# Performance work log

Measured on AMD Instinct MI355X. Metric: run time of the kernel, lower is better.

## Reference

```python
import jax, jax.numpy as jnp
import numpy as np

NS, NC, T, NB = 32, 16, 64, 512
NSC = NS + NC


def setup_inputs() -> dict:
    key = jax.random.key(0)
    k1, k2, k3, k4, k5 = jax.random.split(key, 5)
    # SPD cost matrices so Quu is invertible (as assumed by the LQR math)
    L = jax.random.normal(k1, (NB, T, NSC, NSC), jnp.float32) * 0.1
    Q = L @ jnp.swapaxes(L, -1, -2) + jnp.eye(NSC, dtype=jnp.float32)
    p = jax.random.normal(k2, (NB, T, NSC), jnp.float32)
    x_init = jax.random.normal(k3, (NB, NS), jnp.float32)
    # stable-ish LTI dynamics
    A = 0.9 * jnp.eye(NS, dtype=jnp.float32) + 0.01 * jax.random.normal(k4, (NS, NS), jnp.float32)
    B = 0.1 * jax.random.normal(k5, (NS, NC), jnp.float32)
    dt = jnp.float32(0.1)
    return {"x_init": x_init, "Q": Q, "p": p, "A": A, "B": B, "dt": dt}


def _lqr(x_init, Q, p, A, B):
    ns, nc = A.shape[0], B.shape[1]
    nb, Th = Q.shape[0], Q.shape[1]
    dtype = Q.dtype

    # --- nominal rollout with zero control: x_{t+1} = A x_t ---
    def roll(x, _):
        return x @ A.T, x
    _, cx = jax.lax.scan(roll, x_init, None, length=Th)   # [T,B,ns] states x_0..x_{T-1}
    cu = jnp.zeros((Th, nb, nc), dtype)                    # current_u = 0
    xu = jnp.concatenate([cx, cu], -1)                     # [T,B,nsc]

    Qs = jnp.swapaxes(Q, 0, 1)                             # [T,B,nsc,nsc]
    ps = jnp.swapaxes(p, 0, 1)                             # [T,B,nsc]
    p_new = jnp.einsum('tbij,tbj->tbi', Qs, xu) + ps       # [T,B,nsc]

    F = jnp.concatenate([A, B], axis=1)                    # [ns, nsc]

    # --- backward Riccati recursion (V=v=0 at t=T-1 makes Qt=Q[T-1]) ---
    def bwd(carry, inp):
        V, v = carry                                       # [B,ns,ns], [B,ns]
        Qt_in, qt_in = inp
        Qt = Qt_in + jnp.einsum('si,bst,tj->bij', F, V, F)
        qt = qt_in + v @ F                                 # F^T v
        Qxx, Qxu = Qt[:, :ns, :ns], Qt[:, :ns, ns:]
        Qux, Quu = Qt[:, ns:, :ns], Qt[:, ns:, ns:]
        qx, qu = qt[:, :ns], qt[:, ns:]
        Quu_inv = jnp.linalg.pinv(Quu)
        Kt = -Quu_inv @ Qux                                # [B,nc,ns]
        kt = -jnp.einsum('bij,bj->bi', Quu_inv, qu)        # [B,nc]
        KtT = jnp.swapaxes(Kt, -1, -2)
        Vn = Qxx + Qxu @ Kt + KtT @ Qux + KtT @ Quu @ Kt
        vn = (qx + jnp.einsum('bij,bj->bi', Qxu, kt)
              + jnp.einsum('bij,bj->bi', KtT, qu)
              + jnp.einsum('bij,bj->bi', KtT @ Quu, kt))
        return (Vn, vn), (Kt, kt)

    V0 = jnp.zeros((nb, ns, ns), dtype)
    v0 = jnp.zeros((nb, ns), dtype)
    _, (Ks, ks) = jax.lax.scan(bwd, (V0, v0), (Qs, p_new), reverse=True)

    # --- forward rollout with feedback policy ---
    def fwd(carry, inp):
        xt, cost = carry
        Kt, kt, cxt, cut, Qt, pt = inp
        dut = jnp.einsum('bij,bj->bi', Kt, xt - cxt) + kt
        ut = dut + cut
        xut = jnp.concatenate([xt, ut], -1)
        cost = cost + 0.5 * jnp.einsum('bi,bij,bj->b', xut, Qt, xut) + (xut * pt).sum(-1)
        xn = xt @ A.T + ut @ B.T
        return (xn, cost), (xt, ut)

    (_, cost), (xs, us) = jax.lax.scan(
        fwd, (x_init, jnp.zeros(nb, dtype)), (Ks, ks, cx, cu, Qs, ps))
    x = jnp.swapaxes(xs, 0, 1)   # [B,T,ns]  (states x_0..x_{T-1}, matching x[...,:-1,:])
    u = jnp.swapaxes(us, 0, 1)   # [B,T,nc]
    return x, u, cost


def reference(x_init, Q, p, A, B, dt):
    # dt only matters for nonlinear relinearization; with constant LTI (A,B) it is unused.
    return _lqr(x_init, Q, p, A, B)
```

## Files before the change

kernel.cpp:

```cpp
#include <hip/hip_runtime.h>


#define NSd 32
#define NCd 16
#define Td 64
#define NBd 512
#define NSCd 48
#define SQS 52
#define TP 40

typedef __bf16 bf16x8 __attribute__((ext_vector_type(8)));
typedef __bf16 bf16x4 __attribute__((ext_vector_type(4)));
typedef float f32x4 __attribute__((ext_vector_type(4)));

#define MFMA16(a, b, c) __builtin_amdgcn_mfma_f32_16x16x32_bf16(a, b, c, 0, 0, 0)

#define XOFF ((size_t)0)
#define UOFF ((size_t)NBd * Td * NSd)
#define COFF (UOFF + (size_t)NBd * Td * NCd)

__device__ __forceinline__ float rdl(float v, int l) {
  return __uint_as_float(__builtin_amdgcn_readlane(__float_as_uint(v), l));
}

__device__ __forceinline__ void bar_lgkm() {
  asm volatile("s_waitcnt lgkmcnt(0)\n\ts_barrier" ::: "memory");
}

union LdsU {
  struct {
    __bf16 FTh[48][TP], FTl[48][TP];
    __bf16 Vh[32][TP], Vl[32][TP];
    __bf16 WTh[48][TP], WTl[48][TP];
    __bf16 Xh[32][TP], Xl[32][TP];
    __bf16 KTh[32][TP], KTl[32][TP];
    float Quu[16][17];
    float Qd[3][16][17];
    float qt[48];
    float vv[32];
  } bw;
  struct {
    float K2T[2][16 * 36];
    float kv2[2][16];
    float d[32];
    float xs[32];
    float uu[16];
  } fw;
};

#define SQSTORE(i, v)                            \
  do {                                           \
    int _r = (i) / 12, _c = (i) - _r * 12;       \
    *(float4*)&sQ[_r * SQS + _c * 4] = (v);      \
  } while (0)

__global__ __launch_bounds__(256, 2) void lqr_kernel(
    const float* __restrict__ x_init, const float* __restrict__ Qg,
    const float* __restrict__ pg, const float* __restrict__ Ag,
    const float* __restrict__ Bg, float* __restrict__ out,
    float* __restrict__ wsK, float* __restrict__ wskv) {
  const int b = blockIdx.x;
  const int tid = threadIdx.x;
  const int w = tid >> 6;
  const int lane = tid & 63;
  const int fn = lane & 15;
  const int quad = lane >> 4;
  const int k0 = quad * 8;

  __shared__ __attribute__((aligned(16))) float sQ[48 * SQS];
  __shared__ __attribute__((aligned(16))) float scx[Td][NSd];
  __shared__ __attribute__((aligned(16))) float sFf[NSd][SQS];
  __shared__ __attribute__((aligned(16))) LdsU U;
  __shared__ float scostp[4];

  for (int idx = tid; idx < 1536; idx += 256) {
    int i = idx / 48, j = idx - i * 48;
    sFf[i][j] = (j < 32) ? Ag[i * 32 + j] : Bg[i * 16 + (j - 32)];
  }
  for (int idx = tid; idx < 1536; idx += 256) {
    int a = idx >> 5, k = idx & 31;
    float f = (a < 32) ? Ag[k * 32 + a] : Bg[k * 16 + (a - 32)];
    __bf16 h = (__bf16)f;
    U.bw.FTh[a][k] = h;
    U.bw.FTl[a][k] = (__bf16)(f - (float)h);
  }
  for (int idx = tid; idx < 1024; idx += 256) {
    int r = idx >> 5, c = idx & 31;
    __bf16 z = (__bf16)0.f;
    U.bw.Vh[r][c] = z; U.bw.Vl[r][c] = z;
    U.bw.Xh[r][c] = z; U.bw.Xl[r][c] = z;
    U.bw.KTh[r][c] = z; U.bw.KTl[r][c] = z;
  }
  if (tid < 32) {
    scx[0][tid] = x_init[b * 32 + tid];
    U.bw.vv[tid] = 0.f;
  }
  {
    const float4* src = (const float4*)(Qg + ((size_t)b * Td + 63) * 2304);
    float4 v0 = src[tid];
    float4 v1 = src[tid + 256];
    SQSTORE(tid, v0);
    SQSTORE(tid + 256, v1);
    if (tid < 64) {
      float4 v2 = src[tid + 512];
      SQSTORE(tid + 512, v2);
    }
  }
  float ppf = 0.f;
  if (w == 3 && lane < 48) ppf = pg[((size_t)b * Td + 63) * 48 + lane];
  __syncthreads();

  if (w == 0) {
    for (int t2 = 0; t2 < Td - 1; ++t2) {
      if (lane < 32) {
        float acc = 0.f;
#pragma unroll
        for (int j = 0; j < 32; j += 4) {
          float4 a4 = *(const float4*)&sFf[lane][j];
          acc += a4.x * scx[t2][j] + a4.y * scx[t2][j + 1] +
                 a4.z * scx[t2][j + 2] + a4.w * scx[t2][j + 3];
        }
        scx[t2 + 1][lane] = acc;
      }
    }
  }
  __syncthreads();

  float cAcc = 0.f;
  float dAcc = 0.f;

  for (int t = Td - 1; t >= 0; --t) {
    float4 pf0, pf1, pf2;
    float ppfn;
    if (t > 0) {
      if (w < 3) {
        const float4* src = (const float4*)(Qg + ((size_t)b * Td + (t - 1)) * 2304);
        pf0 = src[tid];
        pf1 = src[tid + 192];
        pf2 = src[tid + 384];
      } else if (lane < 48) {
        ppfn = pg[((size_t)b * Td + t - 1) * 48 + lane];
      }
    }

    if (w < 3) {
      const int I = w;
      bf16x8 aH = *(const bf16x8*)&U.bw.FTh[16 * I + fn][k0];
      bf16x8 aL = *(const bf16x8*)&U.bw.FTl[16 * I + fn][k0];
#pragma unroll
      for (int J = 0; J < 2; ++J) {
        bf16x8 bH = *(const bf16x8*)&U.bw.Vh[16 * J + fn][k0];
        bf16x8 bL = *(const bf16x8*)&U.bw.Vl[16 * J + fn][k0];
        f32x4 acc = {0.f, 0.f, 0.f, 0.f};
        acc = MFMA16(aL, bH, acc);
        acc = MFMA16(aH, bL, acc);
        acc = MFMA16(aH, bH, acc);
#pragma unroll
        for (int r = 0; r < 4; ++r) {
          float v = acc[r];
          __bf16 h = (__bf16)v;
          U.bw.WTh[16 * I + 4 * quad + r][16 * J + fn] = h;
          U.bw.WTl[16 * I + 4 * quad + r][16 * J + fn] = (__bf16)(v - (float)h);
        }
      }
      bf16x8 wH = *(const bf16x8*)&U.bw.WTh[16 * I + fn][k0];
      bf16x8 wL = *(const bf16x8*)&U.bw.WTl[16 * I + fn][k0];
      if (I == 2) {
        bf16x8 bH = *(const bf16x8*)&U.bw.FTh[32 + fn][k0];
        bf16x8 bL = *(const bf16x8*)&U.bw.FTl[32 + fn][k0];
        f32x4 acc;
#pragma unroll
        for (int r = 0; r < 4; ++r)
          acc[r] = sQ[(32 + 4 * quad + r) * SQS + 32 + fn];
        acc = MFMA16(wL, bH, acc);
        acc = MFMA16(wH, bL, acc);
        acc = MFMA16(wH, bH, acc);
#pragma unroll
        for (int r = 0; r < 4; ++r) U.bw.Quu[4 * quad + r][fn] = acc[r];
      } else {
        {
          bf16x8 bH = *(const bf16x8*)&U.bw.FTh[16 * I + fn][k0];
          bf16x8 bL = *(const bf16x8*)&U.bw.FTl[16 * I + fn][k0];
          f32x4 acc;
#pragma unroll
          for (int r = 0; r < 4; ++r)
            acc[r] = sQ[(16 * I + 4 * quad + r) * SQS + 16 * I + fn];
          acc = MFMA16(wL, bH, acc);
          acc = MFMA16(wH, bL, acc);
          acc = MFMA16(wH, bH, acc);
#pragma unroll
          for (int r = 0; r < 4; ++r) U.bw.Qd[I * 2][4 * quad + r][fn] = acc[r];
        }
        if (I == 0) {
          bf16x8 bH = *(const bf16x8*)&U.bw.FTh[16 + fn][k0];
          bf16x8 bL = *(const bf16x8*)&U.bw.FTl[16 + fn][k0];
          f32x4 acc;
#pragma unroll
          for (int r = 0; r < 4; ++r)
            acc[r] = sQ[(4 * quad + r) * SQS + 16 + fn];
          acc = MFMA16(wL, bH, acc);
          acc = MFMA16(wH, bL, acc);
          acc = MFMA16(wH, bH, acc);
#pragma unroll
          for (int r = 0; r < 4; ++r) U.bw.Qd[1][4 * quad + r][fn] = acc[r];
        }
        {
          bf16x8 bH = *(const bf16x8*)&U.bw.FTh[32 + fn][k0];
          bf16x8 bL = *(const bf16x8*)&U.bw.FTl[32 + fn][k0];
          f32x4 acc;
#pragma unroll
          for (int r = 0; r < 4; ++r)
            acc[r] = sQ[(16 * I + 4 * quad + r) * SQS + 32 + fn];
          acc = MFMA16(wL, bH, acc);
          acc = MFMA16(wH, bL, acc);
          acc = MFMA16(wH, bH, acc);
#pragma unroll
          for (int r = 0; r < 4; ++r) {
            float v = acc[r];
            __bf16 h = (__bf16)v;
            U.bw.Xh[16 * I + 4 * quad + r][fn] = h;
            U.bw.Xl[16 * I + 4 * quad + r][fn] = (__bf16)(v - (float)h);
          }
        }
      }
    } else if (lane < 48) {
      float acc1 = ppf;
#pragma unroll
      for (int k = 0; k < 32; ++k) acc1 += sQ[k * SQS + lane] * scx[t][k];
      if (lane < 32) cAcc += 0.5f * scx[t][lane] * (acc1 + ppf);
      float acc = acc1;
#pragma unroll
      for (int k = 0; k < 32; ++k) acc += U.bw.vv[k] * sFf[k][lane];
      U.bw.qt[lane] = acc;
    }
    bar_lgkm();

    if (t > 0) {
      if (w < 3) {
        SQSTORE(tid, pf0);
        SQSTORE(tid + 192, pf1);
        SQSTORE(tid + 384, pf2);
      } else if (lane < 48) {
        ppf = ppfn;
      }
    }
    if (w == 3) {
      float rhs[16];
      if (lane < 32) {
        bf16x8 xh0 = *(const bf16x8*)&U.bw.Xh[lane][0];
        bf16x8 xh1 = *(const bf16x8*)&U.bw.Xh[lane][8];
        bf16x8 xl0 = *(const bf16x8*)&U.bw.Xl[lane][0];
        bf16x8 xl1 = *(const bf16x8*)&U.bw.Xl[lane][8];
#pragma unroll
        for (int i = 0; i < 8; ++i) {
          rhs[i] = (float)xh0[i] + (float)xl0[i];
          rhs[8 + i] = (float)xh1[i] + (float)xl1[i];
        }
      } else {
#pragma unroll
        for (int i = 0; i < 16; ++i) rhs[i] = U.bw.qt[32 + i];
      }
      float quu[16];
#pragma unroll
      for (int i = 0; i < 16; ++i) quu[i] = U.bw.Quu[i][fn];
#pragma unroll
      for (int r = 0; r < 15; ++r) {
        float inv = __builtin_amdgcn_rcpf(rdl(quu[r], r));
#pragma unroll
        for (int i = r + 1; i < 16; ++i) {
          float m = rdl(quu[i], r) * inv;
          rhs[i] -= m * rhs[r];
          quu[i] -= m * quu[r];
        }
      }
      float xx[16];
#pragma unroll
      for (int r = 15; r >= 0; --r) {
        float s = rhs[r];
#pragma unroll
        for (int c = r + 1; c < 16; ++c) s -= rdl(quu[r], c) * xx[c];
        xx[r] = s * __builtin_amdgcn_rcpf(rdl(quu[r], r));
      }
      if (lane < 32) {
        bf16x8 h0, l0, h1, l1;
#pragma unroll
        for (int u = 0; u < 8; ++u) {
          float kv = -xx[u];
          __bf16 hh = (__bf16)kv;
          h0[u] = hh; l0[u] = (__bf16)(kv - (float)hh);
          float kv2 = -xx[8 + u];
          __bf16 hh2 = (__bf16)kv2;
          h1[u] = hh2; l1[u] = (__bf16)(kv2 - (float)hh2);
        }
        *(bf16x8*)&U.bw.KTh[lane][0] = h0;
        *(bf16x8*)&U.bw.KTh[lane][8] = h1;
        *(bf16x8*)&U.bw.KTl[lane][0] = l0;
        *(bf16x8*)&U.bw.KTl[lane][8] = l1;
        float4* dst = (float4*)(wsK + (((size_t)b * Td + t) * 32 + lane) * 16);
        float4 v0 = {-xx[0], -xx[1], -xx[2], -xx[3]};
        float4 v1 = {-xx[4], -xx[5], -xx[6], -xx[7]};
        float4 v2 = {-xx[8], -xx[9], -xx[10], -xx[11]};
        float4 v3 = {-xx[12], -xx[13], -xx[14], -xx[15]};
        dst[0] = v0; dst[1] = v1; dst[2] = v2; dst[3] = v3;
      } else if (lane == 32) {
        float4* dst = (float4*)(wskv + ((size_t)b * Td + t) * 16);
        float4 v0 = {-xx[0], -xx[1], -xx[2], -xx[3]};
        float4 v1 = {-xx[4], -xx[5], -xx[6], -xx[7]};
        float4 v2 = {-xx[8], -xx[9], -xx[10], -xx[11]};
        float4 v3 = {-xx[12], -xx[13], -xx[14], -xx[15]};
        dst[0] = v0; dst[1] = v1; dst[2] = v2; dst[3] = v3;
        float s = 0.f;
#pragma unroll
        for (int i = 0; i < 16; ++i) s += U.bw.qt[32 + i] * xx[i];
        dAcc -= 0.5f * s;
      }
      {
        float acc = 0.f;
        bf16x8 xh0, xh1, xl0, xl1;
        if (lane < 32) {
          xh0 = *(const bf16x8*)&U.bw.Xh[lane][0];
          xh1 = *(const bf16x8*)&U.bw.Xh[lane][8];
          xl0 = *(const bf16x8*)&U.bw.Xl[lane][0];
          xl1 = *(const bf16x8*)&U.bw.Xl[lane][8];
          acc = U.bw.qt[lane];
        }
#pragma unroll
        for (int u = 0; u < 8; ++u) {
          float kt0 = -rdl(xx[u], 32);
          float kt1 = -rdl(xx[8 + u], 32);
          if (lane < 32) {
            acc += ((float)xh0[u] + (float)xl0[u]) * kt0;
            acc += ((float)xh1[u] + (float)xl1[u]) * kt1;
          }
        }
        if (lane < 32) U.bw.vv[lane] = acc;
      }
      {
        bf16x8 aH = *(const bf16x8*)&U.bw.Xh[fn][k0];
        bf16x8 aL = *(const bf16x8*)&U.bw.Xl[fn][k0];
        bf16x8 bH = *(const bf16x8*)&U.bw.KTh[fn][k0];
        bf16x8 bL = *(const bf16x8*)&U.bw.KTl[fn][k0];
        f32x4 acc;
#pragma unroll
        for (int r = 0; r < 4; ++r) acc[r] = U.bw.Qd[0][4 * quad + r][fn];
        acc = MFMA16(aL, bH, acc);
        acc = MFMA16(aH, bL, acc);
        acc = MFMA16(aH, bH, acc);
#pragma unroll
        for (int r = 0; r < 4; ++r) {
          float v = acc[r];
          __bf16 h = (__bf16)v;
          U.bw.Vh[4 * quad + r][fn] = h;
          U.bw.Vl[4 * quad + r][fn] = (__bf16)(v - (float)h);
        }
      }
      {
        bf16x8 aH = *(const bf16x8*)&U.bw.Xh[16 + fn][k0];
        bf16x8 aL = *(const bf16x8*)&U.bw.Xl[16 + fn][k0];
        bf16x8 bH = *(const bf16x8*)&U.bw.KTh[16 + fn][k0];
        bf16x8 bL = *(const bf16x8*)&U.bw.KTl[16 + fn][k0];
        f32x4 acc;
#pragma unroll
        for (int r = 0; r < 4; ++r) acc[r] = U.bw.Qd[2][4 * quad + r][fn];
        acc = MFMA16(aL, bH, acc);
        acc = MFMA16(aH, bL, acc);
        acc = MFMA16(aH, bH, acc);
#pragma unroll
        for (int r = 0; r < 4; ++r) {
          float v = acc[r];
          __bf16 h = (__bf16)v;
          U.bw.Vh[16 + 4 * quad + r][16 + fn] = h;
          U.bw.Vl[16 + 4 * quad + r][16 + fn] = (__bf16)(v - (float)h);
        }
      }
      {
        bf16x8 aH = *(const bf16x8*)&U.bw.Xh[fn][k0];
        bf16x8 aL = *(const bf16x8*)&U.bw.Xl[fn][k0];
        bf16x8 bH = *(const bf16x8*)&U.bw.KTh[16 + fn][k0];
        bf16x8 bL = *(const bf16x8*)&U.bw.KTl[16 + fn][k0];
        f32x4 acc;
#pragma unroll
        for (int r = 0; r < 4; ++r) acc[r] = U.bw.Qd[1][4 * quad + r][fn];
        acc = MFMA16(aL, bH, acc);
        acc = MFMA16(aH, bL, acc);
        acc = MFMA16(aH, bH, acc);
        bf16x4 th, tl;
#pragma unroll
        for (int r = 0; r < 4; ++r) {
          float v = acc[r];
          __bf16 h = (__bf16)v;
          __bf16 l = (__bf16)(v - (float)h);
          U.bw.Vh[4 * quad + r][16 + fn] = h;
          U.bw.Vl[4 * quad + r][16 + fn] = l;
          th[r] = h; tl[r] = l;
        }
        *(bf16x4*)&U.bw.Vh[16 + fn][4 * quad] = th;
        *(bf16x4*)&U.bw.Vl[16 + fn][4 * quad] = tl;
      }
    }
    bar_lgkm();
  }

  if (w == 3) {
    float rv = (lane < 32) ? cAcc : (lane == 32 ? dAcc : 0.f);
    rv += __shfl_down(rv, 32);
    rv += __shfl_down(rv, 16);
    rv += __shfl_down(rv, 8);
    rv += __shfl_down(rv, 4);
    rv += __shfl_down(rv, 2);
    rv += __shfl_down(rv, 1);
    if (lane == 0) scostp[0] = rv;
  }
  __syncthreads();

  if (w == 0) {
    {
      const float4* src = (const float4*)(wsK + ((size_t)b * Td) * 512);
      float4 ka = src[lane * 2], kb = src[lane * 2 + 1];
      int jj = lane >> 1, ib = (lane & 1) * 8;
      float* kt2 = U.fw.K2T[0];
      kt2[(ib + 0) * 36 + jj] = ka.x; kt2[(ib + 1) * 36 + jj] = ka.y;
      kt2[(ib + 2) * 36 + jj] = ka.z; kt2[(ib + 3) * 36 + jj] = ka.w;
      kt2[(ib + 4) * 36 + jj] = kb.x; kt2[(ib + 5) * 36 + jj] = kb.y;
      kt2[(ib + 6) * 36 + jj] = kb.z; kt2[(ib + 7) * 36 + jj] = kb.w;
      if (lane < 16) U.fw.kv2[0][lane] = wskv[(size_t)b * Td * 16 + lane];
    }
    float xr = (lane < 32) ? scx[0][lane] : 0.f;
    for (int t = 0; t < Td; ++t) {
      const int cur = t & 1, nxt = cur ^ 1;
      float4 pa, pb;
      float pk;
      if (t < Td - 1) {
        const float4* src = (const float4*)(wsK + ((size_t)b * Td + t + 1) * 512);
        pa = src[lane * 2];
        pb = src[lane * 2 + 1];
        if (lane < 16) pk = wskv[((size_t)b * Td + t + 1) * 16 + lane];
      }
      if (lane < 32) {
        U.fw.d[lane] = xr - scx[t][lane];
        U.fw.xs[lane] = xr;
        out[XOFF + ((size_t)b * Td + t) * 32 + lane] = xr;
      }
      if (lane < 16) {
        float uv = U.fw.kv2[cur][lane];
        const float* kr = &U.fw.K2T[cur][lane * 36];
#pragma unroll
        for (int j4 = 0; j4 < 8; ++j4) {
          float4 kk = *(const float4*)&kr[j4 * 4];
          float4 dd = *(const float4*)&U.fw.d[j4 * 4];
          uv += kk.x * dd.x + kk.y * dd.y + kk.z * dd.z + kk.w * dd.w;
        }
        U.fw.uu[lane] = uv;
        out[UOFF + ((size_t)b * Td + t) * 16 + lane] = uv;
      }
      if (lane < 32) {
        float acc = 0.f;
#pragma unroll
        for (int j4 = 0; j4 < 8; ++j4) {
          float4 ff = *(const float4*)&sFf[lane][j4 * 4];
          float4 xv = *(const float4*)&U.fw.xs[j4 * 4];
          acc += ff.x * xv.x + ff.y * xv.y + ff.z * xv.z + ff.w * xv.w;
        }
#pragma unroll
        for (int j4 = 0; j4 < 4; ++j4) {
          float4 ff = *(const float4*)&sFf[lane][32 + j4 * 4];
          float4 uv = *(const float4*)&U.fw.uu[j4 * 4];
          acc += ff.x * uv.x + ff.y * uv.y + ff.z * uv.z + ff.w * uv.w;
        }
        xr = acc;
      }
      if (t < Td - 1) {
        int jj = lane >> 1, ib = (lane & 1) * 8;
        float* kt2 = U.fw.K2T[nxt];
        kt2[(ib + 0) * 36 + jj] = pa.x; kt2[(ib + 1) * 36 + jj] = pa.y;
        kt2[(ib + 2) * 36 + jj] = pa.z; kt2[(ib + 3) * 36 + jj] = pa.w;
        kt2[(ib + 4) * 36 + jj] = pb.x; kt2[(ib + 5) * 36 + jj] = pb.y;
        kt2[(ib + 6) * 36 + jj] = pb.z; kt2[(ib + 7) * 36 + jj] = pb.w;
        if (lane < 16) U.fw.kv2[nxt][lane] = pk;
      }
    }
    if (lane == 0) out[COFF + b] = scostp[0];
  }
}

extern "C" void kernel_launch(void* const* d_in, const int* in_sizes, int n_in,
                              void* d_out, int out_size, void* d_ws, size_t ws_size,
                              hipStream_t stream) {
  const float* x_init = (const float*)d_in[0];
  const float* Qg = (const float*)d_in[1];
  const float* pg = (const float*)d_in[2];
  const float* Ag = (const float*)d_in[3];
  const float* Bg = (const float*)d_in[4];
  float* out = (float*)d_out;
  float* wsK = (float*)d_ws;
  float* wskv = wsK + (size_t)NBd * Td * NSd * NCd;
  lqr_kernel<<<NBd, 256, 0, stream>>>(x_init, Qg, pg, Ag, Bg, out, wsK, wskv);
}
```

Baseline: 636.2 us.

## Pack two batch problems per 512-thread block with shared F tables

```diff
diff --git a/kernel.cpp b/kernel.cpp
--- a/kernel.cpp
+++ b/kernel.cpp
@@ -27,100 +27,106 @@
   asm volatile("s_waitcnt lgkmcnt(0)\n\ts_barrier" ::: "memory");
 }
 
-union LdsU {
-  struct {
-    __bf16 FTh[48][TP], FTl[48][TP];
-    __bf16 Vh[32][TP], Vl[32][TP];
-    __bf16 WTh[48][TP], WTl[48][TP];
-    __bf16 Xh[32][TP], Xl[32][TP];
-    __bf16 KTh[32][TP], KTl[32][TP];
-    float Quu[16][17];
-    float Qd[3][16][17];
-    float qt[48];
-    float vv[32];
-  } bw;
-  struct {
-    float K2T[2][16 * 36];
-    float kv2[2][16];
-    float d[32];
-    float xs[32];
-    float uu[16];
-  } fw;
+struct ProbBW {
+  __bf16 Vh[32][TP], Vl[32][TP];
+  __bf16 WTh[48][TP], WTl[48][TP];
+  __bf16 Xh[32][TP], Xl[32][TP];
+  __bf16 KTh[32][TP], KTl[32][TP];
+  float Quu[16][17];
+  float Qd[3][16][17];
+  float qt[48];
+  float vv[32];
 };
-
-#define SQSTORE(i, v)                            \
+struct ProbFW {
+  float K2T[2][16 * 36];
+  float kv2[2][16];
+  float d[32];
+  float xs[32];
+  float uu[16];
+};
+union ProbU {
+  ProbBW bw;
+  ProbFW fw;
+};
+
+#define SQSTORE(base, i, v)                      \
   do {                                           \
     int _r = (i) / 12, _c = (i) - _r * 12;       \
-    *(float4*)&sQ[_r * SQS + _c * 4] = (v);      \
+    *(float4*)&(base)[_r * SQS + _c * 4] = (v);  \
   } while (0)
 
-__global__ __launch_bounds__(256, 2) void lqr_kernel(
+__global__ __launch_bounds__(512, 2) void lqr_kernel(
     const float* __restrict__ x_init, const float* __restrict__ Qg,
     const float* __restrict__ pg, const float* __restrict__ Ag,
     const float* __restrict__ Bg, float* __restrict__ out,
     float* __restrict__ wsK, float* __restrict__ wskv) {
-  const int b = blockIdx.x;
   const int tid = threadIdx.x;
   const int w = tid >> 6;
   const int lane = tid & 63;
+  const int p = w >> 2;
+  const int role = (0x03123210u >> (w * 4)) & 0xF;
+  const int b = blockIdx.x * 2 + p;
+  const int gtid = (w & 3) * 64 + lane;
   const int fn = lane & 15;
   const int quad = lane >> 4;
   const int k0 = quad * 8;
 
-  __shared__ __attribute__((aligned(16))) float sQ[48 * SQS];
-  __shared__ __attribute__((aligned(16))) float scx[Td][NSd];
+  __shared__ __attribute__((aligned(16))) float sQ[2][48 * SQS];
+  __shared__ __attribute__((aligned(16))) float scx[2][Td][NSd];
   __shared__ __attribute__((aligned(16))) float sFf[NSd][SQS];
-  __shared__ __attribute__((aligned(16))) LdsU U;
-  __shared__ float scostp[4];
-
-  for (int idx = tid; idx < 1536; idx += 256) {
+  __shared__ __attribute__((aligned(16))) __bf16 FTh[48][TP];
+  __shared__ __attribute__((aligned(16))) __bf16 FTl[48][TP];
+  __shared__ __attribute__((aligned(16))) ProbU U[2];
+  __shared__ float scostp[2];
+
+  for (int idx = tid; idx < 1536; idx += 512) {
     int i = idx / 48, j = idx - i * 48;
     sFf[i][j] = (j < 32) ? Ag[i * 32 + j] : Bg[i * 16 + (j - 32)];
   }
-  for (int idx = tid; idx < 1536; idx += 256) {
+  for (int idx = tid; idx < 1536; idx += 512) {
     int a = idx >> 5, k = idx & 31;
     float f = (a < 32) ? Ag[k * 32 + a] : Bg[k * 16 + (a - 32)];
     __bf16 h = (__bf16)f;
-    U.bw.FTh[a][k] = h;
-    U.bw.FTl[a][k] = (__bf16)(f - (float)h);
-  }
-  for (int idx = tid; idx < 1024; idx += 256) {
+    FTh[a][k] = h;
+    FTl[a][k] = (__bf16)(f - (float)h);
+  }
+  for (int idx = gtid; idx < 1024; idx += 256) {
     int r = idx >> 5, c = idx & 31;
     __bf16 z = (__bf16)0.f;
-    U.bw.Vh[r][c] = z; U.bw.Vl[r][c] = z;
-    U.bw.Xh[r][c] = z; U.bw.Xl[r][c] = z;
-    U.bw.KTh[r][c] = z; U.bw.KTl[r][c] = z;
-  }
-  if (tid < 32) {
-    scx[0][tid] = x_init[b * 32 + tid];
-    U.bw.vv[tid] = 0.f;
+    U[p].bw.Vh[r][c] = z; U[p].bw.Vl[r][c] = z;
+    U[p].bw.Xh[r][c] = z; U[p].bw.Xl[r][c] = z;
+    U[p].bw.KTh[r][c] = z; U[p].bw.KTl[r][c] = z;
+  }
+  if (gtid < 32) {
+    scx[p][0][gtid] = x_init[b * 32 + gtid];
+    U[p].bw.vv[gtid] = 0.f;
   }
   {
     const float4* src = (const float4*)(Qg + ((size_t)b * Td + 63) * 2304);
-    float4 v0 = src[tid];
-    float4 v1 = src[tid + 256];
-    SQSTORE(tid, v0);
-    SQSTORE(tid + 256, v1);
-    if (tid < 64) {
-      float4 v2 = src[tid + 512];
-      SQSTORE(tid + 512, v2);
+    float4 v0 = src[gtid];
+    float4 v1 = src[gtid + 256];
+    SQSTORE(sQ[p], gtid, v0);
+    SQSTORE(sQ[p], gtid + 256, v1);
+    if (gtid < 64) {
+      float4 v2 = src[gtid + 512];
+      SQSTORE(sQ[p], gtid + 512, v2);
     }
   }
   float ppf = 0.f;
-  if (w == 3 && lane < 48) ppf = pg[((size_t)b * Td + 63) * 48 + lane];
+  if (role == 3 && lane < 48) ppf = pg[((size_t)b * Td + 63) * 48 + lane];
   __syncthreads();
 
-  if (w == 0) {
+  if (role == 0) {
     for (int t2 = 0; t2 < Td - 1; ++t2) {
       if (lane < 32) {
         float acc = 0.f;
 #pragma unroll
         for (int j = 0; j < 32; j += 4) {
           float4 a4 = *(const float4*)&sFf[lane][j];
-          acc += a4.x * scx[t2][j] + a4.y * scx[t2][j + 1] +
-                 a4.z * scx[t2][j + 2] + a4.w * scx[t2][j + 3];
-        }
-        scx[t2 + 1][lane] = acc;
+          acc += a4.x * scx[p][t2][j] + a4.y * scx[p][t2][j + 1] +
+                 a4.z * scx[p][t2][j + 2] + a4.w * scx[p][t2][j + 3];
+        }
+        scx[p][t2 + 1][lane] = acc;
       }
     }
   }
@@ -133,24 +139,25 @@
     float4 pf0, pf1, pf2;
     float ppfn;
     if (t > 0) {
-      if (w < 3) {
+      if (role < 3) {
+        const int ptid = role * 64 + lane;
         const float4* src = (const float4*)(Qg + ((size_t)b * Td + (t - 1)) * 2304);
-        pf0 = src[tid];
-        pf1 = src[tid + 192];
-        pf2 = src[tid + 384];
+        pf0 = src[ptid];
+        pf1 = src[ptid + 192];
+        pf2 = src[ptid + 384];
       } else if (lane < 48) {
         ppfn = pg[((size_t)b * Td + t - 1) * 48 + lane];
       }
     }
 
-    if (w < 3) {
-      const int I = w;
-      bf16x8 aH = *(const bf16x8*)&U.bw.FTh[16 * I + fn][k0];
-      bf16x8 aL = *(const bf16x8*)&U.bw.FTl[16 * I + fn][k0];
+    if (role < 3) {
+      const int I = role;
+      bf16x8 aH = *(const bf16x8*)&FTh[16 * I + fn][k0];
+      bf16x8 aL = *(const bf16x8*)&FTl[16 * I + fn][k0];
 #pragma unroll
       for (int J = 0; J < 2; ++J) {
-        bf16x8 bH = *(const bf16x8*)&U.bw.Vh[16 * J + fn][k0];
-        bf16x8 bL = *(const bf16x8*)&U.bw.Vl[16 * J + fn][k0];
+        bf16x8 bH = *(const bf16x8*)&U[p].bw.Vh[16 * J + fn][k0];
+        bf16x8 bL = *(const bf16x8*)&U[p].bw.Vl[16 * J + fn][k0];
         f32x4 acc = {0.f, 0.f, 0.f, 0.f};
         acc = MFMA16(aL, bH, acc);
         acc = MFMA16(aH, bL, acc);
@@ -159,58 +166,58 @@
         for (int r = 0; r < 4; ++r) {
           float v = acc[r];
           __bf16 h = (__bf16)v;
-          U.bw.WTh[16 * I + 4 * quad + r][16 * J + fn] = h;
-          U.bw.WTl[16 * I + 4 * quad + r][16 * J + fn] = (__bf16)(v - (float)h);
-        }
-      }
-      bf16x8 wH = *(const bf16x8*)&U.bw.WTh[16 * I + fn][k0];
-      bf16x8 wL = *(const bf16x8*)&U.bw.WTl[16 * I + fn][k0];
+          U[p].bw.WTh[16 * I + 4 * quad + r][16 * J + fn] = h;
+          U[p].bw.WTl[16 * I + 4 * quad + r][16 * J + fn] = (__bf16)(v - (float)h);
+        }
+      }
+      bf16x8 wH = *(const bf16x8*)&U[p].bw.WTh[16 * I + fn][k0];
+      bf16x8 wL = *(const bf16x8*)&U[p].bw.WTl[16 * I + fn][k0];
       if (I == 2) {
-        bf16x8 bH = *(const bf16x8*)&U.bw.FTh[32 + fn][k0];
-        bf16x8 bL = *(const bf16x8*)&U.bw.FTl[32 + fn][k0];
+        bf16x8 bH = *(const bf16x8*)&FTh[32 + fn][k0];
+        bf16x8 bL = *(const bf16x8*)&FTl[32 + fn][k0];
         f32x4 acc;
 #pragma unroll
         for (int r = 0; r < 4; ++r)
-          acc[r] = sQ[(32 + 4 * quad + r) * SQS + 32 + fn];
+          acc[r] = sQ[p][(32 + 4 * quad + r) * SQS + 32 + fn];
         acc = MFMA16(wL, bH, acc);
         acc = MFMA16(wH, bL, acc);
         acc = MFMA16(wH, bH, acc);
 #pragma unroll
-        for (int r = 0; r < 4; ++r) U.bw.Quu[4 * quad + r][fn] = acc[r];
+        for (int r = 0; r < 4; ++r) U[p].bw.Quu[4 * quad + r][fn] = acc[r];
       } else {
         {
-          bf16x8 bH = *(const bf16x8*)&U.bw.FTh[16 * I + fn][k0];
-          bf16x8 bL = *(const bf16x8*)&U.bw.FTl[16 * I + fn][k0];
+          bf16x8 bH = *(const bf16x8*)&FTh[16 * I + fn][k0];
+          bf16x8 bL = *(const bf16x8*)&FTl[16 * I + fn][k0];
           f32x4 acc;
 #pragma unroll
           for (int r = 0; r < 4; ++r)
-            acc[r] = sQ[(16 * I + 4 * quad + r) * SQS + 16 * I + fn];
+            acc[r] = sQ[p][(16 * I + 4 * quad + r) * SQS + 16 * I + fn];
           acc = MFMA16(wL, bH, acc);
           acc = MFMA16(wH, bL, acc);
           acc = MFMA16(wH, bH, acc);
 #pragma unroll
-          for (int r = 0; r < 4; ++r) U.bw.Qd[I * 2][4 * quad + r][fn] = acc[r];
+          for (int r = 0; r < 4; ++r) U[p].bw.Qd[I * 2][4 * quad + r][fn] = acc[r];
         }
         if (I == 0) {
-          bf16x8 bH = *(const bf16x8*)&U.bw.FTh[16 + fn][k0];
-          bf16x8 bL = *(const bf16x8*)&U.bw.FTl[16 + fn][k0];
+          bf16x8 bH = *(const bf16x8*)&FTh[16 + fn][k0];
+          bf16x8 bL = *(const bf16x8*)&FTl[16 + fn][k0];
           f32x4 acc;
 #pragma unroll
           for (int r = 0; r < 4; ++r)
-            acc[r] = sQ[(4 * quad + r) * SQS + 16 + fn];
+            acc[r] = sQ[p][(4 * quad + r) * SQS + 16 + fn];
           acc = MFMA16(wL, bH, acc);
           acc = MFMA16(wH, bL, acc);
           acc = MFMA16(wH, bH, acc);
 #pragma unroll
-          for (int r = 0; r < 4; ++r) U.bw.Qd[1][4 * quad + r][fn] = acc[r];
+          for (int r = 0; r < 4; ++r) U[p].bw.Qd[1][4 * quad + r][fn] = acc[r];
         }
         {
-          bf16x8 bH = *(const bf16x8*)&U.bw.FTh[32 + fn][k0];
-          bf16x8 bL = *(const bf16x8*)&U.bw.FTl[32 + fn][k0];
+          bf16x8 bH = *(const bf16x8*)&FTh[32 + fn][k0];
+          bf16x8 bL = *(const bf16x8*)&FTl[32 + fn][k0];
           f32x4 acc;
 #pragma unroll
           for (int r = 0; r < 4; ++r)
-            acc[r] = sQ[(16 * I + 4 * quad + r) * SQS + 32 + fn];
+            acc[r] = sQ[p][(16 * I + 4 * quad + r) * SQS + 32 + fn];
           acc = MFMA16(wL, bH, acc);
           acc = MFMA16(wH, bL, acc);
           acc = MFMA16(wH, bH, acc);
@@ -218,39 +225,40 @@
           for (int r = 0; r < 4; ++r) {
             float v = acc[r];
             __bf16 h = (__bf16)v;
-            U.bw.Xh[16 * I + 4 * quad + r][fn] = h;
-            U.bw.Xl[16 * I + 4 * quad + r][fn] = (__bf16)(v - (float)h);
+            U[p].bw.Xh[16 * I + 4 * quad + r][fn] = h;
+            U[p].bw.Xl[16 * I + 4 * quad + r][fn] = (__bf16)(v - (float)h);
           }
         }
       }
     } else if (lane < 48) {
       float acc1 = ppf;
 #pragma unroll
-      for (int k = 0; k < 32; ++k) acc1 += sQ[k * SQS + lane] * scx[t][k];
-      if (lane < 32) cAcc += 0.5f * scx[t][lane] * (acc1 + ppf);
+      for (int k = 0; k < 32; ++k) acc1 += sQ[p][k * SQS + lane] * scx[p][t][k];
+      if (lane < 32) cAcc += 0.5f * scx[p][t][lane] * (acc1 + ppf);
       float acc = acc1;
 #pragma unroll
-      for (int k = 0; k < 32; ++k) acc += U.bw.vv[k] * sFf[k][lane];
-      U.bw.qt[lane] = acc;
+      for (int k = 0; k < 32; ++k) acc += U[p].bw.vv[k] * sFf[k][lane];
+      U[p].bw.qt[lane] = acc;
     }
     bar_lgkm();
 
     if (t > 0) {
-      if (w < 3) {
-        SQSTORE(tid, pf0);
-        SQSTORE(tid + 192, pf1);
-        SQSTORE(tid + 384, pf2);
+      if (role < 3) {
+        const int ptid = role * 64 + lane;
+        SQSTORE(sQ[p], ptid, pf0);
+        SQSTORE(sQ[p], ptid + 192, pf1);
+        SQSTORE(sQ[p], ptid + 384, pf2);
       } else if (lane < 48) {
         ppf = ppfn;
       }
     }
-    if (w == 3) {
+    if (role == 3) {
       float rhs[16];
       if (lane < 32) {
-        bf16x8 xh0 = *(const bf16x8*)&U.bw.Xh[lane][0];
-        bf16x8 xh1 = *(const bf16x8*)&U.bw.Xh[lane][8];
-        bf16x8 xl0 = *(const bf16x8*)&U.bw.Xl[lane][0];
-        bf16x8 xl1 = *(const bf16x8*)&U.bw.Xl[lane][8];
+        bf16x8 xh0 = *(const bf16x8*)&U[p].bw.Xh[lane][0];
+        bf16x8 xh1 = *(const bf16x8*)&U[p].bw.Xh[lane][8];
+        bf16x8 xl0 = *(const bf16x8*)&U[p].bw.Xl[lane][0];
+        bf16x8 xl1 = *(const bf16x8*)&U[p].bw.Xl[lane][8];
 #pragma unroll
         for (int i = 0; i < 8; ++i) {
           rhs[i] = (float)xh0[i] + (float)xl0[i];
@@ -258,11 +266,11 @@
         }
       } else {
 #pragma unroll
-        for (int i = 0; i < 16; ++i) rhs[i] = U.bw.qt[32 + i];
+        for (int i = 0; i < 16; ++i) rhs[i] = U[p].bw.qt[32 + i];
       }
       float quu[16];
 #pragma unroll
-      for (int i = 0; i < 16; ++i) quu[i] = U.bw.Quu[i][fn];
+      for (int i = 0; i < 16; ++i) quu[i] = U[p].bw.Quu[i][fn];
 #pragma unroll
       for (int r = 0; r < 15; ++r) {
         float inv = __builtin_amdgcn_rcpf(rdl(quu[r], r));
@@ -292,10 +300,10 @@
           __bf16 hh2 = (__bf16)kv2;
           h1[u] = hh2; l1[u] = (__bf16)(kv2 - (float)hh2);
         }
-        *(bf16x8*)&U.bw.KTh[lane][0] = h0;
-        *(bf16x8*)&U.bw.KTh[lane][8] = h1;
-        *(bf16x8*)&U.bw.KTl[lane][0] = l0;
-        *(bf16x8*)&U.bw.KTl[lane][8] = l1;
+        *(bf16x8*)&U[p].bw.KTh[lane][0] = h0;
+        *(bf16x8*)&U[p].bw.KTh[lane][8] = h1;
+        *(bf16x8*)&U[p].bw.KTl[lane][0] = l0;
+        *(bf16x8*)&U[p].bw.KTl[lane][8] = l1;
         float4* dst = (float4*)(wsK + (((size_t)b * Td + t) * 32 + lane) * 16);
         float4 v0 = {-xx[0], -xx[1], -xx[2], -xx[3]};
         float4 v1 = {-xx[4], -xx[5], -xx[6], -xx[7]};
@@ -311,18 +319,18 @@
         dst[0] = v0; dst[1] = v1; dst[2] = v2; dst[3] = v3;
         float s = 0.f;
 #pragma unroll
-        for (int i = 0; i < 16; ++i) s += U.bw.qt[32 + i] * xx[i];
+        for (int i = 0; i < 16; ++i) s += U[p].bw.qt[32 + i] * xx[i];
         dAcc -= 0.5f * s;
       }
       {
         float acc = 0.f;
         bf16x8 xh0, xh1, xl0, xl1;
         if (lane < 32) {
-          xh0 = *(const bf16x8*)&U.bw.Xh[lane][0];
-          xh1 = *(const bf16x8*)&U.bw.Xh[lane][8];
-          xl0 = *(const bf16x8*)&U.bw.Xl[lane][0];
-          xl1 = *(const bf16x8*)&U.bw.Xl[lane][8];
-          acc = U.bw.qt[lane];
+          xh0 = *(const bf16x8*)&U[p].bw.Xh[lane][0];
+          xh1 = *(const bf16x8*)&U[p].bw.Xh[lane][8];
+          xl0 = *(const bf16x8*)&U[p].bw.Xl[lane][0];
+          xl1 = *(const bf16x8*)&U[p].bw.Xl[lane][8];
+          acc = U[p].bw.qt[lane];
         }
 #pragma unroll
         for (int u = 0; u < 8; ++u) {
@@ -333,16 +341,16 @@
             acc += ((float)xh1[u] + (float)xl1[u]) * kt1;
           }
         }
-        if (lane < 32) U.bw.vv[lane] = acc;
+        if (lane < 32) U[p].bw.vv[lane] = acc;
       }
       {
-        bf16x8 aH = *(const bf16x8*)&U.bw.Xh[fn][k0];
-        bf16x8 aL = *(const bf16x8*)&U.bw.Xl[fn][k0];
-        bf16x8 bH = *(const bf16x8*)&U.bw.KTh[fn][k0];
-        bf16x8 bL = *(const bf16x8*)&U.bw.KTl[fn][k0];
+        bf16x8 aH = *(const bf16x8*)&U[p].bw.Xh[fn][k0];
+        bf16x8 aL = *(const bf16x8*)&U[p].bw.Xl[fn][k0];
+        bf16x8 bH = *(const bf16x8*)&U[p].bw.KTh[fn][k0];
+        bf16x8 bL = *(const bf16x8*)&U[p].bw.KTl[fn][k0];
         f32x4 acc;
 #pragma unroll
-        for (int r = 0; r < 4; ++r) acc[r] = U.bw.Qd[0][4 * quad + r][fn];
+        for (int r = 0; r < 4; ++r) acc[r] = U[p].bw.Qd[0][4 * quad + r][fn];
         acc = MFMA16(aL, bH, acc);
         acc = MFMA16(aH, bL, acc);
         acc = MFMA16(aH, bH, acc);
@@ -350,18 +358,18 @@
         for (int r = 0; r < 4; ++r) {
           float v = acc[r];
           __bf16 h = (__bf16)v;
-          U.bw.Vh[4 * quad + r][fn] = h;
-          U.bw.Vl[4 * quad + r][fn] = (__bf16)(v - (float)h);
+          U[p].bw.Vh[4 * quad + r][fn] = h;
+          U[p].bw.Vl[4 * quad + r][fn] = (__bf16)(v - (float)h);
         }
       }
       {
-        bf16x8 aH = *(const bf16x8*)&U.bw.Xh[16 + fn][k0];
-        bf16x8 aL = *(const bf16x8*)&U.bw.Xl[16 + fn][k0];
-        bf16x8 bH = *(const bf16x8*)&U.bw.KTh[16 + fn][k0];
-        bf16x8 bL = *(const bf16x8*)&U.bw.KTl[16 + fn][k0];
+        bf16x8 aH = *(const bf16x8*)&U[p].bw.Xh[16 + fn][k0];
+        bf16x8 aL = *(const bf16x8*)&U[p].bw.Xl[16 + fn][k0];
+        bf16x8 bH = *(const bf16x8*)&U[p].bw.KTh[16 + fn][k0];
+        bf16x8 bL = *(const bf16x8*)&U[p].bw.KTl[16 + fn][k0];
         f32x4 acc;
 #pragma unroll
-        for (int r = 0; r < 4; ++r) acc[r] = U.bw.Qd[2][4 * quad + r][fn];
+        for (int r = 0; r < 4; ++r) acc[r] = U[p].bw.Qd[2][4 * quad + r][fn];
         acc = MFMA16(aL, bH, acc);
         acc = MFMA16(aH, bL, acc);
         acc = MFMA16(aH, bH, acc);
@@ -369,18 +377,18 @@
         for (int r = 0; r < 4; ++r) {
           float v = acc[r];
           __bf16 h = (__bf16)v;
-          U.bw.Vh[16 + 4 * quad + r][16 + fn] = h;
-          U.bw.Vl[16 + 4 * quad + r][16 + fn] = (__bf16)(v - (float)h);
+          U[p].bw.Vh[16 + 4 * quad + r][16 + fn] = h;
+          U[p].bw.Vl[16 + 4 * quad + r][16 + fn] = (__bf16)(v - (float)h);
         }
       }
       {
-        bf16x8 aH = *(const bf16x8*)&U.bw.Xh[fn][k0];
-        bf16x8 aL = *(const bf16x8*)&U.bw.Xl[fn][k0];
-        bf16x8 bH = *(const bf16x8*)&U.bw.KTh[16 + fn][k0];
-        bf16x8 bL = *(const bf16x8*)&U.bw.KTl[16 + fn][k0];
+        bf16x8 aH = *(const bf16x8*)&U[p].bw.Xh[fn][k0];
+        bf16x8 aL = *(const bf16x8*)&U[p].bw.Xl[fn][k0];
+        bf16x8 bH = *(const bf16x8*)&U[p].bw.KTh[16 + fn][k0];
+        bf16x8 bL = *(const bf16x8*)&U[p].bw.KTl[16 + fn][k0];
         f32x4 acc;
 #pragma unroll
-        for (int r = 0; r < 4; ++r) acc[r] = U.bw.Qd[1][4 * quad + r][fn];
+        for (int r = 0; r < 4; ++r) acc[r] = U[p].bw.Qd[1][4 * quad + r][fn];
         acc = MFMA16(aL, bH, acc);
         acc = MFMA16(aH, bL, acc);
         acc = MFMA16(aH, bH, acc);
@@ -390,18 +398,18 @@
           float v = acc[r];
           __bf16 h = (__bf16)v;
           __bf16 l = (__bf16)(v - (float)h);
-          U.bw.Vh[4 * quad + r][16 + fn] = h;
-          U.bw.Vl[4 * quad + r][16 + fn] = l;
+          U[p].bw.Vh[4 * quad + r][16 + fn] = h;
+          U[p].bw.Vl[4 * quad + r][16 + fn] = l;
           th[r] = h; tl[r] = l;
         }
-        *(bf16x4*)&U.bw.Vh[16 + fn][4 * quad] = th;
-        *(bf16x4*)&U.bw.Vl[16 + fn][4 * quad] = tl;
+        *(bf16x4*)&U[p].bw.Vh[16 + fn][4 * quad] = th;
+        *(bf16x4*)&U[p].bw.Vl[16 + fn][4 * quad] = tl;
       }
     }
     bar_lgkm();
   }
 
-  if (w == 3) {
+  if (role == 3) {
     float rv = (lane < 32) ? cAcc : (lane == 32 ? dAcc : 0.f);
     rv += __shfl_down(rv, 32);
     rv += __shfl_down(rv, 16);
@@ -409,23 +417,23 @@
     rv += __shfl_down(rv, 4);
     rv += __shfl_down(rv, 2);
     rv += __shfl_down(rv, 1);
-    if (lane == 0) scostp[0] = rv;
+    if (lane == 0) scostp[p] = rv;
   }
   __syncthreads();
 
-  if (w == 0) {
+  if (role == 0) {
     {
       const float4* src = (const float4*)(wsK + ((size_t)b * Td) * 512);
       float4 ka = src[lane * 2], kb = src[lane * 2 + 1];
       int jj = lane >> 1, ib = (lane & 1) * 8;
-      float* kt2 = U.fw.K2T[0];
+      float* kt2 = U[p].fw.K2T[0];
       kt2[(ib + 0) * 36 + jj] = ka.x; kt2[(ib + 1) * 36 + jj] = ka.y;
       kt2[(ib + 2) * 36 + jj] = ka.z; kt2[(ib + 3) * 36 + jj] = ka.w;
       kt2[(ib + 4) * 36 + jj] = kb.x; kt2[(ib + 5) * 36 + jj] = kb.y;
       kt2[(ib + 6) * 36 + jj] = kb.z; kt2[(ib + 7) * 36 + jj] = kb.w;
-      if (lane < 16) U.fw.kv2[0][lane] = wskv[(size_t)b * Td * 16 + lane];
-    }
-    float xr = (lane < 32) ? scx[0][lane] : 0.f;
+      if (lane < 16) U[p].fw.kv2[0][lane] = wskv[(size_t)b * Td * 16 + lane];
+    }
+    float xr = (lane < 32) ? scx[p][0][lane] : 0.f;
     for (int t = 0; t < Td; ++t) {
       const int cur = t & 1, nxt = cur ^ 1;
       float4 pa, pb;
@@ -437,20 +445,20 @@
         if (lane < 16) pk = wskv[((size_t)b * Td + t + 1) * 16 + lane];
       }
       if (lane < 32) {
-        U.fw.d[lane] = xr - scx[t][lane];
-        U.fw.xs[lane] = xr;
+        U[p].fw.d[lane] = xr - scx[p][t][lane];
+        U[p].fw.xs[lane] = xr;
         out[XOFF + ((size_t)b * Td + t) * 32 + lane] = xr;
       }
       if (lane < 16) {
-        float uv = U.fw.kv2[cur][lane];
-        const float* kr = &U.fw.K2T[cur][lane * 36];
+        float uv = U[p].fw.kv2[cur][lane];
+        const float* kr = &U[p].fw.K2T[cur][lane * 36];
 #pragma unroll
         for (int j4 = 0; j4 < 8; ++j4) {
           float4 kk = *(const float4*)&kr[j4 * 4];
-          float4 dd = *(const float4*)&U.fw.d[j4 * 4];
+          float4 dd = *(const float4*)&U[p].fw.d[j4 * 4];
           uv += kk.x * dd.x + kk.y * dd.y + kk.z * dd.z + kk.w * dd.w;
         }
-        U.fw.uu[lane] = uv;
+        U[p].fw.uu[lane] = uv;
         out[UOFF + ((size_t)b * Td + t) * 16 + lane] = uv;
       }
       if (lane < 32) {
@@ -458,28 +466,28 @@
 #pragma unroll
         for (int j4 = 0; j4 < 8; ++j4) {
           float4 ff = *(const float4*)&sFf[lane][j4 * 4];
-          float4 xv = *(const float4*)&U.fw.xs[j4 * 4];
+          float4 xv = *(const float4*)&U[p].fw.xs[j4 * 4];
           acc += ff.x * xv.x + ff.y * xv.y + ff.z * xv.z + ff.w * xv.w;
         }
 #pragma unroll
         for (int j4 = 0; j4 < 4; ++j4) {
           float4 ff = *(const float4*)&sFf[lane][32 + j4 * 4];
-          float4 uv = *(const float4*)&U.fw.uu[j4 * 4];
+          float4 uv = *(const float4*)&U[p].fw.uu[j4 * 4];
           acc += ff.x * uv.x + ff.y * uv.y + ff.z * uv.z + ff.w * uv.w;
         }
         xr = acc;
       }
       if (t < Td - 1) {
         int jj = lane >> 1, ib = (lane & 1) * 8;
-        float* kt2 = U.fw.K2T[nxt];
+        float* kt2 = U[p].fw.K2T[nxt];
         kt2[(ib + 0) * 36 + jj] = pa.x; kt2[(ib + 1) * 36 + jj] = pa.y;
         kt2[(ib + 2) * 36 + jj] = pa.z; kt2[(ib + 3) * 36 + jj] = pa.w;
         kt2[(ib + 4) * 36 + jj] = pb.x; kt2[(ib + 5) * 36 + jj] = pb.y;
         kt2[(ib + 6) * 36 + jj] = pb.z; kt2[(ib + 7) * 36 + jj] = pb.w;
-        if (lane < 16) U.fw.kv2[nxt][lane] = pk;
-      }
-    }
-    if (lane == 0) out[COFF + b] = scostp[0];
+        if (lane < 16) U[p].fw.kv2[nxt][lane] = pk;
+      }
+    }
+    if (lane == 0) out[COFF + b] = scostp[p];
   }
 }
 
@@ -494,5 +502,5 @@
   float* out = (float*)d_out;
   float* wsK = (float*)d_ws;
   float* wskv = wsK + (size_t)NBd * Td * NSd * NCd;
-  lqr_kernel<<<NBd, 256, 0, stream>>>(x_init, Qg, pg, Ag, Bg, out, wsK, wskv);
+  lqr_kernel<<<NBd / 2, 512, 0, stream>>>(x_init, Qg, pg, Ag, Bg, out, wsK, wskv);
 }
```

Result: slower. 652.3 us (+2.5%).
